# Kernel optimization log

Measured on AMD Instinct MI355X. Metric: run time of the kernel, lower is better.

Reference implementation:

```python
import jax, jax.numpy as jnp
import numpy as np

NUM_PERIODS = 24


def setup_inputs() -> dict:
    key = jax.random.key(0)
    ks = jax.random.split(key, 12)
    B, N, F, H, E = 32, 1024, 128, 64, 16
    scale = 1.0 / np.sqrt(F)
    inp = {
        "input_features": jax.random.normal(ks[0], (B, N, F), jnp.float32),
        "cycle_indices": jax.random.randint(ks[1], (B,), 0, NUM_PERIODS, jnp.int64),
        "weight": jax.random.normal(ks[2], (F, F), jnp.float32) * scale,
        "bias": jnp.zeros((F,), jnp.float32),
        "src_emb": jax.random.normal(ks[3], (NUM_PERIODS, N, H), jnp.float32) * 0.1,
        "tgt_emb": jax.random.normal(ks[4], (NUM_PERIODS, N, H), jnp.float32) * 0.1,
        "env_W": jax.random.normal(ks[5], (E, H), jnp.float32) * (1.0 / np.sqrt(E)),
        "env_b": jnp.zeros((H,), jnp.float32),
        "res_W": jax.random.normal(ks[6], (F, F), jnp.float32) * scale,
        "res_b": jnp.zeros((F,), jnp.float32),
        "static_adj": (jax.random.uniform(ks[7], (N, N)) < 0.05).astype(jnp.float32),
        "env_features": jax.random.normal(ks[8], (N, E), jnp.float32),
    }
    return inp


def reference(input_features, cycle_indices, weight, bias, src_emb, tgt_emb,
              env_W, env_b, res_W, res_b, static_adj, env_features):
    # env encoder: Linear + ReLU (dropout is identity at inference)
    env_emb = jax.nn.relu(env_features @ env_W + env_b)            # [N, H]

    # per-period adaptive adjacency, masked by static sparsity pattern
    src = src_emb + env_emb                                        # [P, N, H]
    tgt = tgt_emb + env_emb                                        # [P, N, H]
    scores = jnp.einsum('pnh,pmh->pnm', src, tgt)                  # [P, N, N]
    adj = jax.nn.relu(scores) * static_adj                         # [P, N, N]

    period = (cycle_indices % NUM_PERIODS).astype(jnp.int32)       # [B]
    adj_b = adj[period]                                            # [B, N, N]

    support = jnp.einsum('bnd,dm->bnm', input_features, weight)    # [B, N, F]
    convolved = jnp.einsum('bnm,bmf->bnf', adj_b, support) + bias  # [B, N, F]

    residual = jax.nn.relu(input_features @ res_W + res_b)         # [B, N, F]
    return jax.nn.relu(convolved + residual)
```

## Files before the change

### kernel.cpp

```cpp
#include <hip/hip_runtime.h>
#include <hip/hip_bf16.h>

#define NPER 24
#define B_ 32
#define N_ 1024
#define F_ 128
#define H_ 64
#define E_ 16

typedef __attribute__((ext_vector_type(8))) short short8;
typedef __attribute__((ext_vector_type(4))) float f32x4;

#define GLD16(g, l) __builtin_amdgcn_global_load_lds( \
    (const __attribute__((address_space(1))) void*)(g), \
    (__attribute__((address_space(3))) void*)(l), 16, 0, 0)

static __device__ __forceinline__ unsigned short f2bf(float x) {
    union { float f; unsigned u; } v; v.f = x;
    unsigned r = v.u + 0x7fffu + ((v.u >> 16) & 1u);
    return (unsigned short)(r >> 16);
}
static __device__ __forceinline__ float bf2f(unsigned short h) {
    union { unsigned u; float f; } v; v.u = ((unsigned)h) << 16; return v.f;
}
static __device__ __forceinline__ unsigned short f2bf_hw(float x) {
    __hip_bfloat16 h = __float2bfloat16(x);
    return *(unsigned short*)&h;
}

__global__ __launch_bounds__(256) void prep_all(
    const float* __restrict__ src_emb, const float* __restrict__ tgt_emb,
    const float* __restrict__ env_features, const float* __restrict__ env_W,
    const float* __restrict__ env_b,
    const float* __restrict__ adj, const float* __restrict__ W,
    const float* __restrict__ rW,
    unsigned short* __restrict__ src_bf, unsigned short* __restrict__ tgt_bf,
    unsigned short* __restrict__ adj_bf, unsigned short* __restrict__ Wt,
    unsigned short* __restrict__ rWt)
{
    const int bid = blockIdx.x;
    if (bid < 256) {
        const int idx = bid * 256 + threadIdx.x;
        const int n = idx >> 6, h = idx & 63;
        float e = env_b[h];
#pragma unroll
        for (int k = 0; k < E_; ++k)
            e = fmaf(env_features[n * E_ + k], env_W[k * H_ + h], e);
        e = fmaxf(e, 0.f);
#pragma unroll 4
        for (int p = 0; p < NPER; ++p) {
            const size_t off = (size_t)p * (N_ * H_) + idx;
            src_bf[off] = f2bf(src_emb[off] + e);
            tgt_bf[off] = f2bf(tgt_emb[off] + e);
        }
    } else if (bid < 1280) {
        const size_t i = ((size_t)(bid - 256) * 256 + threadIdx.x) * 4;
        float4 v = *(const float4*)(adj + i);
        ushort4 o;
        o.x = f2bf(v.x); o.y = f2bf(v.y); o.z = f2bf(v.z); o.w = f2bf(v.w);
        *(ushort4*)(adj_bf + i) = o;
    } else {
        const int idx = (bid - 1280) * 256 + threadIdx.x;
        const int which = idx >> 14, j = idx & 16383;
        const int f = j >> 7, d = j & 127;
        if (which == 0) Wt[f * 128 + d]  = f2bf(W[d * 128 + f]);
        else            rWt[f * 128 + d] = f2bf(rW[d * 128 + f]);
    }
}

__global__ __launch_bounds__(256) void gemm2_mfma(
    const float* __restrict__ x,
    const unsigned short* __restrict__ Wt,
    const unsigned short* __restrict__ rWt,
    const float* __restrict__ rb,
    unsigned short* __restrict__ supT,
    unsigned short* __restrict__ resid)
{
    const int t = threadIdx.x, w = t >> 6, l = t & 63;
    const int ln = l & 15, kb = l >> 4;
    const int mblk = w >> 1, fhalf = w & 1;
    const int row0 = blockIdx.x * 32;
    const int b   = row0 >> 10;
    const int mg0 = row0 & 1023;

    const float* xrow = x + (size_t)(row0 + mblk * 16 + ln) * 128;
    short8 xa[4];
#pragma unroll
    for (int k = 0; k < 4; ++k) {
        float4 v0 = *(const float4*)(xrow + k * 32 + kb * 8);
        float4 v1 = *(const float4*)(xrow + k * 32 + kb * 8 + 4);
        short8 s;
        s[0] = (short)f2bf(v0.x); s[1] = (short)f2bf(v0.y);
        s[2] = (short)f2bf(v0.z); s[3] = (short)f2bf(v0.w);
        s[4] = (short)f2bf(v1.x); s[5] = (short)f2bf(v1.y);
        s[6] = (short)f2bf(v1.z); s[7] = (short)f2bf(v1.w);
        xa[k] = s;
    }

    f32x4 accS[4], accR[4];
#pragma unroll
    for (int i = 0; i < 4; ++i) { accS[i] = (f32x4){0,0,0,0}; accR[i] = (f32x4){0,0,0,0}; }

#pragma unroll
    for (int k = 0; k < 4; ++k) {
#pragma unroll
        for (int fb = 0; fb < 4; ++fb) {
            int fr = (fhalf * 4 + fb) * 16 + ln;
            short8 wa = *(const short8*)(Wt  + (size_t)fr * 128 + k * 32 + kb * 8);
            short8 wb = *(const short8*)(rWt + (size_t)fr * 128 + k * 32 + kb * 8);
            accS[fb] = __builtin_amdgcn_mfma_f32_16x16x32_bf16(wa, xa[k], accS[fb], 0, 0, 0);
            accR[fb] = __builtin_amdgcn_mfma_f32_16x16x32_bf16(xa[k], wb, accR[fb], 0, 0, 0);
        }
    }

#pragma unroll
    for (int fb = 0; fb < 4; ++fb) {
        int m = mg0 + mblk * 16 + ln;
#pragma unroll
        for (int i = 0; i < 4; ++i) {
            int f = (fhalf * 4 + fb) * 16 + kb * 4 + i;
            supT[((size_t)b * 128 + f) * 1024 + m] = f2bf(accS[fb][i]);
        }
    }
#pragma unroll
    for (int fb = 0; fb < 4; ++fb) {
        int f = (fhalf * 4 + fb) * 16 + ln;
        float rbf = rb[f];
#pragma unroll
        for (int i = 0; i < 4; ++i) {
            size_t row = (size_t)row0 + mblk * 16 + kb * 4 + i;
            resid[row * 128 + f] = f2bf(fmaxf(accR[fb][i] + rbf, 0.f));
        }
    }
}

__global__ __launch_bounds__(256, 2) void conv_mfma(
    const unsigned short* __restrict__ src_bf,
    const unsigned short* __restrict__ tgt_bf,
    const unsigned short* __restrict__ adj_bf,
    const unsigned short* __restrict__ supT,
    const unsigned short* __restrict__ resid,
    const float* __restrict__ bias,
    const int* __restrict__ cyc,
    float* __restrict__ out)
{
    __shared__ unsigned short s_tgt[2][64 * 64] __attribute__((aligned(16)));
    __shared__ unsigned short s_sup[2][128 * 64] __attribute__((aligned(16)));
    __shared__ unsigned short s_a[64][72] __attribute__((aligned(16)));

    const int i = blockIdx.x;
    const int work = (i & 7) * 64 + (i >> 3);
    const int b  = work >> 4;
    const int n0 = (work & 15) * 64;

    const int t = threadIdx.x, w = t >> 6, l = t & 63;
    const int ln = l & 15, kb = l >> 4;
    const int p = ((cyc[b] % NPER) + NPER) % NPER;

    const int sn = w >> 1, sm = w & 1;
    const int cf = w;

    short8 sfrag[2][2];
#pragma unroll
    for (int nt = 0; nt < 2; ++nt)
#pragma unroll
        for (int k2 = 0; k2 < 2; ++k2)
            sfrag[nt][k2] = *(const short8*)(
                src_bf + ((size_t)p * N_ + n0 + sn * 32 + nt * 16 + ln) * H_ + k2 * 32 + kb * 8);

    const unsigned short* tgtg = tgt_bf + (size_t)p * N_ * H_;
    const unsigned short* supg = supT + (size_t)b * F_ * N_;

    f32x4 acc[4][2];
#pragma unroll
    for (int q = 0; q < 4; ++q)
#pragma unroll
        for (int fb = 0; fb < 2; ++fb) acc[q][fb] = (f32x4){0, 0, 0, 0};

    auto stage = [&](int buf, int m0) {
#pragma unroll
        for (int j = 0; j < 2; ++j) {
            const int te = j * 256 + t;
            const int r = te >> 3, c = te & 7;
            GLD16(tgtg + (size_t)(m0 + r) * H_ + (c ^ (r & 7)) * 8,
                  &s_tgt[buf][te * 8]);
        }
#pragma unroll
        for (int j = 0; j < 4; ++j) {
            const int te = j * 256 + t;
            const int r = te >> 3, c = te & 7;
            GLD16(supg + (size_t)r * N_ + m0 + (c ^ (r & 7)) * 8,
                  &s_sup[buf][te * 8]);
        }
    };

    auto loadAdj = [&](int m0, ushort4 (&av)[2][2]) {
#pragma unroll
        for (int nt = 0; nt < 2; ++nt)
#pragma unroll
            for (int mt = 0; mt < 2; ++mt)
                av[nt][mt] = *(const ushort4*)(
                    adj_bf + (size_t)(n0 + sn * 32 + nt * 16 + ln) * N_
                           + m0 + sm * 32 + mt * 16 + kb * 4);
    };

    auto score = [&](int buf, const ushort4 (&av)[2][2]) {
        short8 tf[2][2];
#pragma unroll
        for (int mt = 0; mt < 2; ++mt)
#pragma unroll
            for (int k2 = 0; k2 < 2; ++k2) {
                const int trow = sm * 32 + mt * 16 + ln;
                tf[mt][k2] = *(const short8*)(
                    &s_tgt[buf][trow * 64 + ((k2 * 4 + kb) ^ (ln & 7)) * 8]);
            }
#pragma unroll
        for (int nt = 0; nt < 2; ++nt)
#pragma unroll
            for (int mt = 0; mt < 2; ++mt) {
                f32x4 c = (f32x4){0, 0, 0, 0};
                c = __builtin_amdgcn_mfma_f32_16x16x32_bf16(tf[mt][0], sfrag[nt][0], c, 0, 0, 0);
                c = __builtin_amdgcn_mfma_f32_16x16x32_bf16(tf[mt][1], sfrag[nt][1], c, 0, 0, 0);
                const int nl = sn * 32 + nt * 16 + ln;
                const int ml = sm * 32 + mt * 16 + kb * 4;
                const ushort4 a = av[nt][mt];
                uint2 q;
                q.x = (unsigned)f2bf_hw(fmaxf(c[0], 0.f) * bf2f(a.x))
                    | ((unsigned)f2bf_hw(fmaxf(c[1], 0.f) * bf2f(a.y)) << 16);
                q.y = (unsigned)f2bf_hw(fmaxf(c[2], 0.f) * bf2f(a.z))
                    | ((unsigned)f2bf_hw(fmaxf(c[3], 0.f) * bf2f(a.w)) << 16);
                *(uint2*)(&s_a[nl][ml]) = q;
            }
    };

    auto conv = [&](int buf) {
#pragma unroll
        for (int ks = 0; ks < 2; ++ks) {
            short8 bfrag[2];
#pragma unroll
            for (int fb = 0; fb < 2; ++fb) {
                const int frow = cf * 32 + fb * 16 + ln;
                bfrag[fb] = *(const short8*)(
                    &s_sup[buf][frow * 64 + ((ks * 4 + kb) ^ (ln & 7)) * 8]);
            }
#pragma unroll
            for (int nt2 = 0; nt2 < 4; ++nt2) {
                short8 af = *(const short8*)(&s_a[nt2 * 16 + ln][ks * 32 + kb * 8]);
#pragma unroll
                for (int fb = 0; fb < 2; ++fb)
                    acc[nt2][fb] = __builtin_amdgcn_mfma_f32_16x16x32_bf16(
                        af, bfrag[fb], acc[nt2][fb], 0, 0, 0);
            }
        }
    };

    auto bar_lgkm = []() {
        asm volatile("s_waitcnt lgkmcnt(0)" ::: "memory");
        __builtin_amdgcn_s_barrier();
    };
    auto bar_vm0 = []() {
        asm volatile("s_waitcnt vmcnt(0) lgkmcnt(0)" ::: "memory");
        __builtin_amdgcn_s_barrier();
    };

    ushort4 avA[2][2], avB[2][2];

    stage(0, 0);
    loadAdj(0, avA);
    bar_vm0();

    for (int tt = 0; tt < 16; tt += 2) {
        stage(1, (tt + 1) * 64);
        loadAdj((tt + 1) * 64, avB);
        score(0, avA);
        bar_lgkm();
        conv(0);
        bar_vm0();

        if (tt + 2 < 16) {
            stage(0, (tt + 2) * 64);
            loadAdj((tt + 2) * 64, avA);
        }
        score(1, avB);
        bar_lgkm();
        conv(1);
        bar_vm0();
    }

#pragma unroll
    for (int nt2 = 0; nt2 < 4; ++nt2)
#pragma unroll
    for (int fb = 0; fb < 2; ++fb) {
        const int f = cf * 32 + fb * 16 + ln;
        const float bi = bias[f];
#pragma unroll
        for (int ii = 0; ii < 4; ++ii) {
            const int n = n0 + nt2 * 16 + kb * 4 + ii;
            const size_t o = ((size_t)b * N_ + n) * F_ + f;
            out[o] = fmaxf(acc[nt2][fb][ii] + bi + bf2f(resid[o]), 0.f);
        }
    }
}

extern "C" void kernel_launch(void* const* d_in, const int* in_sizes, int n_in,
                              void* d_out, int out_size, void* d_ws, size_t ws_size,
                              hipStream_t stream) {
    const float* input_features = (const float*)d_in[0];
    const int*   cycle_indices  = (const int*)  d_in[1];
    const float* weight         = (const float*)d_in[2];
    const float* bias           = (const float*)d_in[3];
    const float* src_emb        = (const float*)d_in[4];
    const float* tgt_emb        = (const float*)d_in[5];
    const float* env_W          = (const float*)d_in[6];
    const float* env_b          = (const float*)d_in[7];
    const float* res_W          = (const float*)d_in[8];
    const float* res_b          = (const float*)d_in[9];
    const float* static_adj     = (const float*)d_in[10];
    const float* env_features   = (const float*)d_in[11];
    float* out = (float*)d_out;

    char* wsb = (char*)d_ws;
    unsigned short* src_bf = (unsigned short*)wsb;
    unsigned short* tgt_bf = src_bf + (size_t)NPER * N_ * H_;
    unsigned short* Wt     = tgt_bf + (size_t)NPER * N_ * H_;
    unsigned short* rWt    = Wt + 16384;
    unsigned short* supT   = rWt + 16384;
    unsigned short* resid  = supT + (size_t)B_ * F_ * N_;
    unsigned short* adj_bf = resid + (size_t)B_ * N_ * F_;

    prep_all<<<1408, 256, 0, stream>>>(
        src_emb, tgt_emb, env_features, env_W, env_b,
        static_adj, weight, res_W,
        src_bf, tgt_bf, adj_bf, Wt, rWt);

    gemm2_mfma<<<(B_ * N_) / 32, 256, 0, stream>>>(
        input_features, Wt, rWt, res_b, supT, resid);

    conv_mfma<<<512, 256, 0, stream>>>(
        src_bf, tgt_bf, adj_bf, supT, resid, bias, cycle_indices, out);
}
```

Baseline: 64.11 us.

## Stage weights in LDS for projection GEMM and pre-convert inputs to bf16

The projection GEMM now loads both transposed weight matrices and a 64-row x tile into LDS via global_load_lds with an XOR swizzle. Each wave computes all 128 output columns for its 16 rows, so weights are reused from LDS instead of being re-read from global memory. Input features are converted to bf16 in the prep kernel, and the prep work for the embeddings is spread over more blocks. The swizzle index in the conv kernel changes from lane-based to row-based. The costs are an extra full pass writing and reading x in bf16 and 80KB of LDS per block.

```diff
diff --git a/kernel.cpp b/kernel.cpp
--- a/kernel.cpp
+++ b/kernel.cpp
@@ -33,103 +33,118 @@
     const float* __restrict__ env_features, const float* __restrict__ env_W,
     const float* __restrict__ env_b,
     const float* __restrict__ adj, const float* __restrict__ W,
-    const float* __restrict__ rW,
+    const float* __restrict__ rW, const float* __restrict__ x,
     unsigned short* __restrict__ src_bf, unsigned short* __restrict__ tgt_bf,
     unsigned short* __restrict__ adj_bf, unsigned short* __restrict__ Wt,
-    unsigned short* __restrict__ rWt)
+    unsigned short* __restrict__ rWt, unsigned short* __restrict__ x_bf)
 {
     const int bid = blockIdx.x;
-    if (bid < 256) {
-        const int idx = bid * 256 + threadIdx.x;
+    if (bid < 1536) {
+        const int g   = bid >> 8;
+        const int idx = (bid & 255) * 256 + threadIdx.x;
         const int n = idx >> 6, h = idx & 63;
         float e = env_b[h];
 #pragma unroll
         for (int k = 0; k < E_; ++k)
             e = fmaf(env_features[n * E_ + k], env_W[k * H_ + h], e);
         e = fmaxf(e, 0.f);
-#pragma unroll 4
-        for (int p = 0; p < NPER; ++p) {
-            const size_t off = (size_t)p * (N_ * H_) + idx;
+#pragma unroll
+        for (int pp = 0; pp < 4; ++pp) {
+            const size_t off = (size_t)(g * 4 + pp) * (N_ * H_) + idx;
             src_bf[off] = f2bf(src_emb[off] + e);
             tgt_bf[off] = f2bf(tgt_emb[off] + e);
         }
-    } else if (bid < 1280) {
-        const size_t i = ((size_t)(bid - 256) * 256 + threadIdx.x) * 4;
+    } else if (bid < 2560) {
+        const size_t i = ((size_t)(bid - 1536) * 256 + threadIdx.x) * 4;
         float4 v = *(const float4*)(adj + i);
         ushort4 o;
         o.x = f2bf(v.x); o.y = f2bf(v.y); o.z = f2bf(v.z); o.w = f2bf(v.w);
         *(ushort4*)(adj_bf + i) = o;
-    } else {
-        const int idx = (bid - 1280) * 256 + threadIdx.x;
+    } else if (bid < 2688) {
+        const int idx = (bid - 2560) * 256 + threadIdx.x;
         const int which = idx >> 14, j = idx & 16383;
         const int f = j >> 7, d = j & 127;
         if (which == 0) Wt[f * 128 + d]  = f2bf(W[d * 128 + f]);
         else            rWt[f * 128 + d] = f2bf(rW[d * 128 + f]);
-    }
-}
-
-__global__ __launch_bounds__(256) void gemm2_mfma(
-    const float* __restrict__ x,
+    } else {
+        const size_t i = ((size_t)(bid - 2688) * 256 + threadIdx.x) * 4;
+        float4 v = *(const float4*)(x + i);
+        ushort4 o;
+        o.x = f2bf(v.x); o.y = f2bf(v.y); o.z = f2bf(v.z); o.w = f2bf(v.w);
+        *(ushort4*)(x_bf + i) = o;
+    }
+}
+
+__global__ __launch_bounds__(256, 2) void gemm2_mfma(
+    const unsigned short* __restrict__ x_bf,
     const unsigned short* __restrict__ Wt,
     const unsigned short* __restrict__ rWt,
     const float* __restrict__ rb,
     unsigned short* __restrict__ supT,
     unsigned short* __restrict__ resid)
 {
+    __shared__ unsigned short s_w[128 * 128] __attribute__((aligned(16)));
+    __shared__ unsigned short s_r[128 * 128] __attribute__((aligned(16)));
+    __shared__ unsigned short s_x[64 * 128]  __attribute__((aligned(16)));
+
     const int t = threadIdx.x, w = t >> 6, l = t & 63;
     const int ln = l & 15, kb = l >> 4;
-    const int mblk = w >> 1, fhalf = w & 1;
-    const int row0 = blockIdx.x * 32;
-    const int b   = row0 >> 10;
-    const int mg0 = row0 & 1023;
-
-    const float* xrow = x + (size_t)(row0 + mblk * 16 + ln) * 128;
-    short8 xa[4];
+    const size_t row0 = (size_t)blockIdx.x * 64;
+    const int b   = (int)(row0 >> 10);
+    const int mg0 = (int)(row0 & 1023);
+
+#pragma unroll
+    for (int j = 0; j < 8; ++j) {
+        const int te = j * 256 + t;
+        const int r = te >> 4, c = te & 15;
+        GLD16(Wt  + (size_t)r * 128 + (c ^ (r & 7)) * 8, &s_w[te * 8]);
+        GLD16(rWt + (size_t)r * 128 + (c ^ (r & 7)) * 8, &s_r[te * 8]);
+    }
+#pragma unroll
+    for (int j = 0; j < 4; ++j) {
+        const int te = j * 256 + t;
+        const int r = te >> 4, c = te & 15;
+        GLD16(x_bf + row0 * 128 + (size_t)r * 128 + (c ^ (r & 7)) * 8,
+              &s_x[te * 8]);
+    }
+    asm volatile("s_waitcnt vmcnt(0) lgkmcnt(0)" ::: "memory");
+    __builtin_amdgcn_s_barrier();
+
+    f32x4 accS[8], accR[8];
+#pragma unroll
+    for (int q = 0; q < 8; ++q) { accS[q] = (f32x4){0,0,0,0}; accR[q] = (f32x4){0,0,0,0}; }
+
+    const int xr = w * 16 + ln;
 #pragma unroll
     for (int k = 0; k < 4; ++k) {
-        float4 v0 = *(const float4*)(xrow + k * 32 + kb * 8);
-        float4 v1 = *(const float4*)(xrow + k * 32 + kb * 8 + 4);
-        short8 s;
-        s[0] = (short)f2bf(v0.x); s[1] = (short)f2bf(v0.y);
-        s[2] = (short)f2bf(v0.z); s[3] = (short)f2bf(v0.w);
-        s[4] = (short)f2bf(v1.x); s[5] = (short)f2bf(v1.y);
-        s[6] = (short)f2bf(v1.z); s[7] = (short)f2bf(v1.w);
-        xa[k] = s;
-    }
-
-    f32x4 accS[4], accR[4];
-#pragma unroll
-    for (int i = 0; i < 4; ++i) { accS[i] = (f32x4){0,0,0,0}; accR[i] = (f32x4){0,0,0,0}; }
-
-#pragma unroll
-    for (int k = 0; k < 4; ++k) {
-#pragma unroll
-        for (int fb = 0; fb < 4; ++fb) {
-            int fr = (fhalf * 4 + fb) * 16 + ln;
-            short8 wa = *(const short8*)(Wt  + (size_t)fr * 128 + k * 32 + kb * 8);
-            short8 wb = *(const short8*)(rWt + (size_t)fr * 128 + k * 32 + kb * 8);
-            accS[fb] = __builtin_amdgcn_mfma_f32_16x16x32_bf16(wa, xa[k], accS[fb], 0, 0, 0);
-            accR[fb] = __builtin_amdgcn_mfma_f32_16x16x32_bf16(xa[k], wb, accR[fb], 0, 0, 0);
-        }
-    }
-
-#pragma unroll
-    for (int fb = 0; fb < 4; ++fb) {
-        int m = mg0 + mblk * 16 + ln;
+        short8 xa = *(const short8*)(&s_x[xr * 128 + ((k * 4 + kb) ^ (xr & 7)) * 8]);
+#pragma unroll
+        for (int ff = 0; ff < 8; ++ff) {
+            const int fr = ff * 16 + ln;
+            short8 wa = *(const short8*)(&s_w[fr * 128 + ((k * 4 + kb) ^ (fr & 7)) * 8]);
+            short8 wb = *(const short8*)(&s_r[fr * 128 + ((k * 4 + kb) ^ (fr & 7)) * 8]);
+            accS[ff] = __builtin_amdgcn_mfma_f32_16x16x32_bf16(wa, xa, accS[ff], 0, 0, 0);
+            accR[ff] = __builtin_amdgcn_mfma_f32_16x16x32_bf16(xa, wb, accR[ff], 0, 0, 0);
+        }
+    }
+
+#pragma unroll
+    for (int ff = 0; ff < 8; ++ff) {
+        const int m = mg0 + w * 16 + ln;
 #pragma unroll
         for (int i = 0; i < 4; ++i) {
-            int f = (fhalf * 4 + fb) * 16 + kb * 4 + i;
-            supT[((size_t)b * 128 + f) * 1024 + m] = f2bf(accS[fb][i]);
-        }
-    }
-#pragma unroll
-    for (int fb = 0; fb < 4; ++fb) {
-        int f = (fhalf * 4 + fb) * 16 + ln;
-        float rbf = rb[f];
+            const int f = ff * 16 + kb * 4 + i;
+            supT[((size_t)b * 128 + f) * 1024 + m] = f2bf(accS[ff][i]);
+        }
+    }
+#pragma unroll
+    for (int ff = 0; ff < 8; ++ff) {
+        const int f = ff * 16 + ln;
+        const float rbf = rb[f];
 #pragma unroll
         for (int i = 0; i < 4; ++i) {
-            size_t row = (size_t)row0 + mblk * 16 + kb * 4 + i;
-            resid[row * 128 + f] = f2bf(fmaxf(accR[fb][i] + rbf, 0.f));
+            const size_t row = row0 + w * 16 + kb * 4 + i;
+            resid[row * 128 + f] = f2bf(fmaxf(accR[ff][i] + rbf, 0.f));
         }
     }
 }
@@ -212,7 +227,7 @@
             for (int k2 = 0; k2 < 2; ++k2) {
                 const int trow = sm * 32 + mt * 16 + ln;
                 tf[mt][k2] = *(const short8*)(
-                    &s_tgt[buf][trow * 64 + ((k2 * 4 + kb) ^ (ln & 7)) * 8]);
+                    &s_tgt[buf][trow * 64 + ((k2 * 4 + kb) ^ (trow & 7)) * 8]);
             }
 #pragma unroll
         for (int nt = 0; nt < 2; ++nt)
@@ -241,7 +256,7 @@
             for (int fb = 0; fb < 2; ++fb) {
                 const int frow = cf * 32 + fb * 16 + ln;
                 bfrag[fb] = *(const short8*)(
-                    &s_sup[buf][frow * 64 + ((ks * 4 + kb) ^ (ln & 7)) * 8]);
+                    &s_sup[buf][frow * 64 + ((ks * 4 + kb) ^ (frow & 7)) * 8]);
             }
 #pragma unroll
             for (int nt2 = 0; nt2 < 4; ++nt2) {
@@ -327,14 +342,15 @@
     unsigned short* supT   = rWt + 16384;
     unsigned short* resid  = supT + (size_t)B_ * F_ * N_;
     unsigned short* adj_bf = resid + (size_t)B_ * N_ * F_;
-
-    prep_all<<<1408, 256, 0, stream>>>(
+    unsigned short* x_bf   = adj_bf + (size_t)N_ * N_;
+
+    prep_all<<<6784, 256, 0, stream>>>(
         src_emb, tgt_emb, env_features, env_W, env_b,
-        static_adj, weight, res_W,
-        src_bf, tgt_bf, adj_bf, Wt, rWt);
-
-    gemm2_mfma<<<(B_ * N_) / 32, 256, 0, stream>>>(
-        input_features, Wt, rWt, res_b, supT, resid);
+        static_adj, weight, res_W, input_features,
+        src_bf, tgt_bf, adj_bf, Wt, rWt, x_bf);
+
+    gemm2_mfma<<<(B_ * N_) / 64, 256, 0, stream>>>(
+        x_bf, Wt, rWt, res_b, supT, resid);
 
     conv_mfma<<<512, 256, 0, stream>>>(
         src_bf, tgt_bf, adj_bf, supT, resid, bias, cycle_indices, out);
```

After: 54.58 us, median of 2. -14.9%, faster.
